# Kernel optimization log

Measured on AMD Instinct MI355X. Metric: run time of the kernel, lower is better.

The kernel has to match this reference:

```python
import jax, jax.numpy as jnp
import numpy as np

EPS = 1e-5


def _bn(x, g, b):
    # training-mode BatchNorm2d over (N, H, W), biased variance
    m = jnp.mean(x, axis=(0, 2, 3), keepdims=True)
    v = jnp.var(x, axis=(0, 2, 3), keepdims=True)
    return (x - m) * jax.lax.rsqrt(v + EPS) * g[None, :, None, None] + b[None, :, None, None]


def _conv1x1(x, w):
    # x: [B, Cin, H, W], w: [Cout, Cin]
    return jnp.einsum('bchw,oc->bohw', x, w)


def _prop_attention(x, wq, wkv, wo, bo, obj_dict, bg_dict, rand_inds):
    B, C, H, W = x.shape  # B == 1
    heads, crop = rand_inds.shape[0], rand_inds.shape[1]
    dh = C // heads
    HW = H * W
    num_obj = crop // 2
    # original does x.clone().detach() before attention
    xd = jax.lax.stop_gradient(x)
    xh = xd.reshape(heads, dh, HW)  # batch=1 folded away (matches t.view(-1, crop**2))
    # pos[h, i, j] = flat pixel index gathered for head h, group i, slot j
    pos = jnp.concatenate(
        [obj_dict[rand_inds[:, :num_obj]], bg_dict[rand_inds[:, num_obj:]]], axis=1
    )  # [heads, crop, crop]
    tokens = jax.vmap(lambda xv, pv: xv[:, pv])(xh, pos)  # [heads, dh, crop, crop]
    tokens = tokens.transpose(0, 2, 3, 1).reshape(heads * crop, crop, dh)
    q = tokens @ wq.T
    k, v = jnp.split(tokens @ wkv.T, 2, axis=-1)
    dots = jnp.einsum('bie,bje->bij', q, k) * (dh ** -0.5)
    attn = jax.nn.softmax(dots, axis=-1)
    out = jnp.einsum('bij,bje->bie', attn, v)  # [heads*crop, crop, dh]
    # faithful to torch out.view(heads*crop, -1, crop): a raw row-major reinterpret
    out_r = out.reshape(heads, crop, dh, crop)
    vals = out_r.transpose(0, 2, 1, 3).reshape(heads, dh, crop * crop)
    pos_flat = pos.reshape(heads, crop * crop)
    # pos is a bijection onto [0, HW) per head -> invert and gather
    ar = jnp.arange(HW, dtype=jnp.int32)
    inv = jax.vmap(lambda p: jnp.zeros((HW,), jnp.int32).at[p].set(ar))(pos_flat)
    img = jax.vmap(lambda vh, ih: vh[:, ih])(vals, inv)  # [heads, dh, HW]
    img = img.reshape(1, heads * dh, H, W)
    # to_out: Linear(dim, dim) applied channels-last
    return jnp.einsum('bchw,oc->bohw', img, wo) + bo[None, :, None, None]


def setup_inputs():
    H = W = 300
    HW = H * W
    heads, crop = 2, H
    num_obj = crop // 2
    ch, emb = 256, 64
    dh = emb // heads
    key = jax.random.key(0)
    ks = jax.random.split(key, 10)
    x = jax.random.normal(ks[0], (1, ch, H, W), jnp.float32)
    perm = jax.random.permutation(ks[1], HW)
    obj_dict = perm[: HW // 2]
    bg_dict = perm[HW // 2 :]
    ri = []
    for h in range(heads):
        po = jax.random.permutation(jax.random.fold_in(ks[2], h), HW // 2).reshape(num_obj, crop)
        pb = jax.random.permutation(jax.random.fold_in(ks[3], h), HW // 2).reshape(crop - num_obj, crop)
        ri.append(jnp.concatenate([po, pb], axis=0))
    rand_inds = jnp.stack(ri)  # [heads, crop, crop]
    w_conv1 = jax.random.normal(ks[4], (emb, ch), jnp.float32) / np.sqrt(ch)
    wq = jax.random.normal(ks[5], (dh, dh), jnp.float32) / np.sqrt(dh)
    wkv = jax.random.normal(ks[6], (2 * dh, dh), jnp.float32) / np.sqrt(dh)
    wo = jax.random.normal(ks[7], (emb, emb), jnp.float32) / np.sqrt(emb)
    bo = jnp.zeros((emb,), jnp.float32)
    w_conv2 = jax.random.normal(ks[8], (emb, 2 * emb), jnp.float32) / np.sqrt(2 * emb)
    return {
        'x': x,
        'w_conv1': w_conv1,
        'bn1_g': jnp.ones((emb,), jnp.float32),
        'bn1_b': jnp.zeros((emb,), jnp.float32),
        'wq': wq,
        'wkv': wkv,
        'wo': wo,
        'bo': bo,
        'w_conv2': w_conv2,
        'bn2_g': jnp.ones((emb,), jnp.float32),
        'bn2_b': jnp.zeros((emb,), jnp.float32),
        'obj_dict': obj_dict,
        'bg_dict': bg_dict,
        'rand_inds': rand_inds,
    }


def reference(x, w_conv1, bn1_g, bn1_b, wq, wkv, wo, bo, w_conv2, bn2_g, bn2_b, obj_dict, bg_dict, rand_inds):
    x1 = jax.nn.relu(_bn(_conv1x1(x, w_conv1), bn1_g, bn1_b))
    xa = jax.nn.relu(_prop_attention(x1, wq, wkv, wo, bo, obj_dict, bg_dict, rand_inds))
    xc = jnp.concatenate([xa, x1], axis=1)
    return jax.nn.relu(_bn(_conv1x1(xc, w_conv2), bn2_g, bn2_b))
```

## Files before the change

kernel.cpp:

```cpp
#include <hip/hip_runtime.h>
#include <hip/hip_bf16.h>

#define HW 90000
#define CROP 300
#define C2EXP 0.25503492f

typedef __attribute__((ext_vector_type(8))) short s8v;
typedef __attribute__((ext_vector_type(4))) float f4v;
#define MFMA16(a,b,c) __builtin_amdgcn_mfma_f32_16x16x32_bf16(a,b,c,0,0,0)

__device__ __forceinline__ unsigned short f2bf(float f) {
    unsigned int u = __float_as_uint(f);
    return (unsigned short)((u + 0x7fffu + ((u >> 16) & 1u)) >> 16);
}
__device__ __forceinline__ float bf2f(unsigned short s) {
    return __uint_as_float(((unsigned int)s) << 16);
}
__device__ __forceinline__ s8v pack8(float4 u0, float4 u1) {
    s8v A;
    A[0] = (short)f2bf(u0.x); A[1] = (short)f2bf(u0.y);
    A[2] = (short)f2bf(u0.z); A[3] = (short)f2bf(u0.w);
    A[4] = (short)f2bf(u1.x); A[5] = (short)f2bf(u1.y);
    A[6] = (short)f2bf(u1.z); A[7] = (short)f2bf(u1.w);
    return A;
}

__global__ void prep_kernel(const float* __restrict__ w1, const float* __restrict__ wq,
                            const float* __restrict__ wkv, const float* __restrict__ wo,
                            const float* __restrict__ w2,
                            short* __restrict__ w1b, short* __restrict__ wqb,
                            short* __restrict__ wkvb, short* __restrict__ wob,
                            short* __restrict__ w2b) {
    int idx = blockIdx.x * blockDim.x + threadIdx.x;
    int stride = gridDim.x * blockDim.x;
    for (int i = idx; i < 16384; i += stride) w1b[i] = (short)f2bf(w1[i]);
    for (int i = idx; i < 1024; i += stride)  wqb[i] = (short)f2bf(wq[i]);
    for (int i = idx; i < 2048; i += stride)  wkvb[i] = (short)f2bf(wkv[i]);
    for (int i = idx; i < 4096; i += stride)  wob[i] = (short)f2bf(wo[i]);
    for (int i = idx; i < 8192; i += stride)  w2b[i] = (short)f2bf(w2[i]);
}

__global__ __launch_bounds__(256, 2) void conv1_mfma(const float* __restrict__ x,
        const short* __restrict__ w1b, float* __restrict__ y1t, float* __restrict__ stat) {
    const int wave = threadIdx.x >> 6, lane = threadIdx.x & 63;
    const int q = lane >> 4, n = lane & 15;
    const int tile = blockIdx.x * 4 + wave;
    const int s0 = tile * 16;
    s8v B[8][4];
#pragma unroll
    for (int kb = 0; kb < 8; ++kb)
#pragma unroll
        for (int nt = 0; nt < 4; ++nt)
            B[kb][nt] = *(const s8v*)(w1b + (nt * 16 + n) * 256 + kb * 32 + q * 8);
    f4v acc[4];
#pragma unroll
    for (int nt = 0; nt < 4; ++nt) acc[nt] = f4v{0.f, 0.f, 0.f, 0.f};
    if (s0 < HW) {
#pragma unroll
        for (int kb = 0; kb < 8; ++kb) {
            float a8[8];
#pragma unroll
            for (int j = 0; j < 8; ++j)
                a8[j] = x[(size_t)(kb * 32 + q * 8 + j) * HW + s0 + n];
            s8v A;
#pragma unroll
            for (int j = 0; j < 8; ++j) A[j] = (short)f2bf(a8[j]);
#pragma unroll
            for (int nt = 0; nt < 4; ++nt) acc[nt] = MFMA16(A, B[kb][nt], acc[nt]);
        }
#pragma unroll
        for (int nt = 0; nt < 4; ++nt)
#pragma unroll
            for (int r = 0; r < 4; ++r)
                y1t[(size_t)(s0 + q * 4 + r) * 64 + nt * 16 + n] = acc[nt][r];
    }
    float s1[4], s2[4];
#pragma unroll
    for (int nt = 0; nt < 4; ++nt) {
        s1[nt] = acc[nt][0] + acc[nt][1] + acc[nt][2] + acc[nt][3];
        s2[nt] = acc[nt][0]*acc[nt][0] + acc[nt][1]*acc[nt][1]
               + acc[nt][2]*acc[nt][2] + acc[nt][3]*acc[nt][3];
    }
#pragma unroll
    for (int m = 16; m < 64; m <<= 1)
#pragma unroll
        for (int nt = 0; nt < 4; ++nt) {
            s1[nt] += __shfl_xor(s1[nt], m, 64);
            s2[nt] += __shfl_xor(s2[nt], m, 64);
        }
    __shared__ float red[2][4][64];
    if (lane < 16)
#pragma unroll
        for (int nt = 0; nt < 4; ++nt) {
            red[0][wave][nt * 16 + lane] = s1[nt];
            red[1][wave][nt * 16 + lane] = s2[nt];
        }
    __syncthreads();
    if (threadIdx.x < 128) {
        int k = threadIdx.x >> 6, c = threadIdx.x & 63;
        atomicAdd(&stat[k * 64 + c],
                  red[k][0][c] + red[k][1][c] + red[k][2][c] + red[k][3][c]);
    }
}

__global__ void bn_fin_kernel(const float* __restrict__ stat,
        const float* __restrict__ g, const float* __restrict__ b, float* __restrict__ ab) {
    int c = threadIdx.x;
    float m = stat[c] * (1.f / HW);
    float v = stat[64 + c] * (1.f / HW) - m * m;
    float ac = g[c] * rsqrtf(v + 1e-5f);
    ab[c] = ac;
    ab[64 + c] = b[c] - m * ac;
}

__global__ __launch_bounds__(512, 4) void attn_mfma_kernel(const float* __restrict__ y1t,
        const float* __restrict__ ab1,
        const short* __restrict__ wqb, const short* __restrict__ wkvb,
        const int* __restrict__ obj, const int* __restrict__ bg,
        const int* __restrict__ rinds, float* __restrict__ img) {
    __shared__ __align__(16) short tokQ[304 * 40];
    __shared__ __align__(16) short kbuf[304 * 40];
    __shared__ __align__(16) short vt[32 * 328];
    __shared__ __align__(16) short pbuf[8 * 16 * 40];
    __shared__ int possh[304];
    const int b = blockIdx.x;
    const int h = b / CROP, i = b - h * CROP;
    const int tid = threadIdx.x;
    const int wave = tid >> 6, lane = tid & 63, q = lane >> 4, n = lane & 15;

    const float4 a4 = *(const float4*)(ab1 + h * 32 + (tid & 7) * 4);
    const float4 b4 = *(const float4*)(ab1 + 64 + h * 32 + (tid & 7) * 4);

    if (tid < 300) {
        int ri = rinds[h * HW + i * CROP + tid];
        possh[tid] = (i < 150) ? obj[ri] : bg[ri];
    } else if (tid < 380) {
        ((unsigned int*)(tokQ + 300 * 40))[tid - 300] = 0;
    } else if (tid < 460) {
        ((unsigned int*)(kbuf + 300 * 40))[tid - 380] = 0;
    }
    for (int ii = tid; ii < 320; ii += 512) {
        int e = ii / 10, w = ii - 10 * e;
        ((unsigned int*)vt)[e * 164 + 150 + w] = 0;
    }
    __syncthreads();

    for (int idx = tid; idx < 2400; idx += 512) {
        int j = idx >> 3, part = idx & 7;
        float4 v = *(const float4*)(y1t + (size_t)possh[j] * 64 + h * 32 + part * 4);
        v.x = fmaxf(fmaf(a4.x, v.x, b4.x), 0.f);
        v.y = fmaxf(fmaf(a4.y, v.y, b4.y), 0.f);
        v.z = fmaxf(fmaf(a4.z, v.z, b4.z), 0.f);
        v.w = fmaxf(fmaf(a4.w, v.w, b4.w), 0.f);
        uint2 pk;
        pk.x = (unsigned int)f2bf(v.x) | ((unsigned int)f2bf(v.y) << 16);
        pk.y = (unsigned int)f2bf(v.z) | ((unsigned int)f2bf(v.w) << 16);
        *(uint2*)(tokQ + j * 40 + part * 4) = pk;
    }
    __syncthreads();

    {
        s8v bq0 = *(const s8v*)(wqb + n * 32 + q * 8);
        s8v bq1 = *(const s8v*)(wqb + (16 + n) * 32 + q * 8);
        s8v bk0 = *(const s8v*)(wkvb + n * 32 + q * 8);
        s8v bk1 = *(const s8v*)(wkvb + (16 + n) * 32 + q * 8);
        s8v bv0 = *(const s8v*)(wkvb + (32 + n) * 32 + q * 8);
        s8v bv1 = *(const s8v*)(wkvb + (48 + n) * 32 + q * 8);
        f4v zz = {0.f, 0.f, 0.f, 0.f};
#pragma unroll
        for (int ti = 0; ti < 3; ++ti) {
            int t = wave + ti * 8;
            if (t < 19) {
                s8v at = *(const s8v*)(tokQ + (16 * t + n) * 40 + q * 8);
                f4v qf0 = MFMA16(at, bq0, zz);
                f4v qf1 = MFMA16(at, bq1, zz);
                f4v kf0 = MFMA16(at, bk0, zz);
                f4v kf1 = MFMA16(at, bk1, zz);
                f4v vf0 = MFMA16(at, bv0, zz);
                f4v vf1 = MFMA16(at, bv1, zz);
#pragma unroll
                for (int r = 0; r < 4; ++r) {
                    int row = 16 * t + q * 4 + r;
                    tokQ[row * 40 + n]      = (short)f2bf(qf0[r]);
                    tokQ[row * 40 + 16 + n] = (short)f2bf(qf1[r]);
                    kbuf[row * 40 + n]      = (short)f2bf(kf0[r]);
                    kbuf[row * 40 + 16 + n] = (short)f2bf(kf1[r]);
                    vt[n * 328 + row]        = (short)f2bf(vf0[r]);
                    vt[(16 + n) * 328 + row] = (short)f2bf(vf1[r]);
                }
            }
        }
    }
    __syncthreads();

    s8v aQ[3];
#pragma unroll
    for (int ti = 0; ti < 3; ++ti) {
        int t = wave + ti * 8;
        aQ[ti] = (t < 19) ? *(const s8v*)(tokQ + (16 * t + n) * 40 + q * 8) : s8v{};
    }
    __syncthreads();

    f4v O[3][2];
    float lsum[3][4];
#pragma unroll
    for (int ti = 0; ti < 3; ++ti) {
        O[ti][0] = f4v{0.f, 0.f, 0.f, 0.f};
        O[ti][1] = f4v{0.f, 0.f, 0.f, 0.f};
#pragma unroll
        for (int r = 0; r < 4; ++r) lsum[ti][r] = 0.f;
    }
    short* pw = pbuf + wave * 16 * 40;
    f4v zz = {0.f, 0.f, 0.f, 0.f};
    for (int kb = 0; kb < 10; ++kb) {
        const int key0 = kb * 32 + n;
        const int key1 = kb * 32 + 16 + n;
        s8v bV0 = *(const s8v*)(vt + n * 328 + kb * 32 + q * 8);
        s8v bV1 = *(const s8v*)(vt + (16 + n) * 328 + kb * 32 + q * 8);
        s8v bK0 = *(const s8v*)(kbuf + key0 * 40 + q * 8);
        int r1 = key1 < 304 ? key1 : 303;
        s8v bK1 = *(const s8v*)(kbuf + r1 * 40 + q * 8);
#pragma unroll
        for (int ti = 0; ti < 3; ++ti) {
            int t = wave + ti * 8;
            if (t >= 19) continue;
            f4v s0 = MFMA16(aQ[ti], bK0, zz);
            f4v s1 = MFMA16(aQ[ti], bK1, zz);
#pragma unroll
            for (int r = 0; r < 4; ++r) {
                float e0 = (key0 < 300) ? exp2f(s0[r] * C2EXP) : 0.f;
                float e1 = (key1 < 300) ? exp2f(s1[r] * C2EXP) : 0.f;
                unsigned short p0 = f2bf(e0), p1 = f2bf(e1);
                lsum[ti][r] += bf2f(p0) + bf2f(p1);
                pw[(q * 4 + r) * 40 + n]      = (short)p0;
                pw[(q * 4 + r) * 40 + 16 + n] = (short)p1;
            }
            asm volatile("s_waitcnt lgkmcnt(0)" ::: "memory");
            s8v ap = *(const s8v*)(pw + n * 40 + q * 8);
            O[ti][0] = MFMA16(ap, bV0, O[ti][0]);
            O[ti][1] = MFMA16(ap, bV1, O[ti][1]);
        }
    }

#pragma unroll
    for (int m = 1; m < 16; m <<= 1) {
#pragma unroll
        for (int ti = 0; ti < 3; ++ti)
#pragma unroll
            for (int r = 0; r < 4; ++r)
                lsum[ti][r] += __shfl_xor(lsum[ti][r], m, 64);
    }
    short* outb = tokQ;
#pragma unroll
    for (int ti = 0; ti < 3; ++ti) {
        int t = wave + ti * 8;
        if (t >= 19) continue;
#pragma unroll
        for (int r = 0; r < 4; ++r) {
            float rl = 1.f / lsum[ti][r];
            int row = 16 * t + q * 4 + r;
            outb[row * 32 + n]      = (short)f2bf(O[ti][0][r] * rl);
            outb[row * 32 + 16 + n] = (short)f2bf(O[ti][1][r] * rl);
        }
    }
    __syncthreads();

    for (int idx = tid; idx < 9600; idx += 512) {
        int jj = idx >> 5, dd = idx & 31;
        img[(size_t)possh[jj] * 64 + h * 32 + dd] = bf2f((unsigned short)outb[dd * CROP + jj]);
    }
}

__global__ __launch_bounds__(256, 2) void fuse2_mfma(const float* __restrict__ img,
        const float* __restrict__ y1t, const float* __restrict__ ab1,
        const short* __restrict__ wob, const short* __restrict__ w2b,
        const float* __restrict__ bo, float* __restrict__ y2, float* __restrict__ stat) {
    __shared__ __align__(16) short xas[4][16 * 72];
    __shared__ float ytr[64 * 133];
    __shared__ float red[2][4][64];
    const int wave = threadIdx.x >> 6, lane = threadIdx.x & 63;
    const int q = lane >> 4, n = lane & 15;
    s8v Bo[2][4], B2[4][4];
#pragma unroll
    for (int kb = 0; kb < 2; ++kb)
#pragma unroll
        for (int nt = 0; nt < 4; ++nt)
            Bo[kb][nt] = *(const s8v*)(wob + (nt * 16 + n) * 64 + kb * 32 + q * 8);
#pragma unroll
    for (int kb = 0; kb < 4; ++kb)
#pragma unroll
        for (int nt = 0; nt < 4; ++nt)
            B2[kb][nt] = *(const s8v*)(w2b + (nt * 16 + n) * 128 + kb * 32 + q * 8);
    float4 a1v[2][2], b1v[2][2];
#pragma unroll
    for (int kb = 0; kb < 2; ++kb)
#pragma unroll
        for (int hh = 0; hh < 2; ++hh) {
            a1v[kb][hh] = *(const float4*)(ab1 + kb * 32 + q * 8 + hh * 4);
            b1v[kb][hh] = *(const float4*)(ab1 + 64 + kb * 32 + q * 8 + hh * 4);
        }
    float bov[4];
#pragma unroll
    for (int nt = 0; nt < 4; ++nt) bov[nt] = bo[nt * 16 + n];

    float s1[4] = {0.f, 0.f, 0.f, 0.f}, s2[4] = {0.f, 0.f, 0.f, 0.f};
    short* xw = xas[wave];
#pragma unroll
    for (int ti = 0; ti < 2; ++ti) {
        int tile = blockIdx.x * 8 + wave * 2 + ti;
        if (tile >= 5625) continue;
        int s0 = tile * 16;
        f4v xacc[4];
#pragma unroll
        for (int nt = 0; nt < 4; ++nt) xacc[nt] = f4v{0.f, 0.f, 0.f, 0.f};
#pragma unroll
        for (int kb = 0; kb < 2; ++kb) {
            const float4* ip = (const float4*)(img + (size_t)(s0 + n) * 64 + kb * 32 + q * 8);
            s8v A = pack8(ip[0], ip[1]);
#pragma unroll
            for (int nt = 0; nt < 4; ++nt) xacc[nt] = MFMA16(A, Bo[kb][nt], xacc[nt]);
        }
#pragma unroll
        for (int nt = 0; nt < 4; ++nt)
#pragma unroll
            for (int r = 0; r < 4; ++r) {
                float v = fmaxf(xacc[nt][r] + bov[nt], 0.f);
                xw[(q * 4 + r) * 72 + nt * 16 + n] = (short)f2bf(v);
            }
        asm volatile("s_waitcnt lgkmcnt(0)" ::: "memory");
        f4v yacc[4];
#pragma unroll
        for (int nt = 0; nt < 4; ++nt) yacc[nt] = f4v{0.f, 0.f, 0.f, 0.f};
#pragma unroll
        for (int kb = 0; kb < 2; ++kb) {
            s8v Axa = *(const s8v*)(xw + n * 72 + kb * 32 + q * 8);
#pragma unroll
            for (int nt = 0; nt < 4; ++nt) yacc[nt] = MFMA16(Axa, B2[kb][nt], yacc[nt]);
        }
#pragma unroll
        for (int kb = 0; kb < 2; ++kb) {
            const float4* yp = (const float4*)(y1t + (size_t)(s0 + n) * 64 + kb * 32 + q * 8);
            float4 u0 = yp[0], u1 = yp[1];
            u0.x = fmaxf(fmaf(a1v[kb][0].x, u0.x, b1v[kb][0].x), 0.f);
            u0.y = fmaxf(fmaf(a1v[kb][0].y, u0.y, b1v[kb][0].y), 0.f);
            u0.z = fmaxf(fmaf(a1v[kb][0].z, u0.z, b1v[kb][0].z), 0.f);
            u0.w = fmaxf(fmaf(a1v[kb][0].w, u0.w, b1v[kb][0].w), 0.f);
            u1.x = fmaxf(fmaf(a1v[kb][1].x, u1.x, b1v[kb][1].x), 0.f);
            u1.y = fmaxf(fmaf(a1v[kb][1].y, u1.y, b1v[kb][1].y), 0.f);
            u1.z = fmaxf(fmaf(a1v[kb][1].z, u1.z, b1v[kb][1].z), 0.f);
            u1.w = fmaxf(fmaf(a1v[kb][1].w, u1.w, b1v[kb][1].w), 0.f);
            s8v A = pack8(u0, u1);
#pragma unroll
            for (int nt = 0; nt < 4; ++nt) yacc[nt] = MFMA16(A, B2[kb + 2][nt], yacc[nt]);
        }
        int pl = wave * 32 + ti * 16;
#pragma unroll
        for (int nt = 0; nt < 4; ++nt)
#pragma unroll
            for (int r = 0; r < 4; ++r) {
                float v = yacc[nt][r];
                s1[nt] += v; s2[nt] += v * v;
                ytr[(nt * 16 + n) * 133 + pl + q * 4 + r] = v;
            }
    }
#pragma unroll
    for (int m = 16; m < 64; m <<= 1)
#pragma unroll
        for (int nt = 0; nt < 4; ++nt) {
            s1[nt] += __shfl_xor(s1[nt], m, 64);
            s2[nt] += __shfl_xor(s2[nt], m, 64);
        }
    if (lane < 16)
#pragma unroll
        for (int nt = 0; nt < 4; ++nt) {
            red[0][wave][nt * 16 + lane] = s1[nt];
            red[1][wave][nt * 16 + lane] = s2[nt];
        }
    __syncthreads();
    int s0b = blockIdx.x * 128;
    for (int i = threadIdx.x; i < 8192; i += 256) {
        int c = i >> 7, p = i & 127;
        int s = s0b + p;
        if (s < HW) y2[(size_t)c * HW + s] = ytr[c * 133 + p];
    }
    if (threadIdx.x < 128) {
        int k = threadIdx.x >> 6, c = threadIdx.x & 63;
        atomicAdd(&stat[k * 64 + c],
                  red[k][0][c] + red[k][1][c] + red[k][2][c] + red[k][3][c]);
    }
}

__global__ __launch_bounds__(256) void bn_out_kernel(const float* __restrict__ y2,
        const float* __restrict__ ab2, float* __restrict__ out) {
    int c = blockIdx.y;
    int s4 = blockIdx.x * 256 + threadIdx.x;
    if (s4 >= 22500) return;
    float a = ab2[c], b = ab2[64 + c];
    float4 v = *(const float4*)(y2 + (size_t)c * HW + s4 * 4);
    v.x = fmaxf(fmaf(a, v.x, b), 0.f);
    v.y = fmaxf(fmaf(a, v.y, b), 0.f);
    v.z = fmaxf(fmaf(a, v.z, b), 0.f);
    v.w = fmaxf(fmaf(a, v.w, b), 0.f);
    *(float4*)(out + (size_t)c * HW + s4 * 4) = v;
}

extern "C" void kernel_launch(void* const* d_in, const int* in_sizes, int n_in,
                              void* d_out, int out_size, void* d_ws, size_t ws_size,
                              hipStream_t stream) {
    const float* x   = (const float*)d_in[0];
    const float* w1  = (const float*)d_in[1];
    const float* g1  = (const float*)d_in[2];
    const float* b1  = (const float*)d_in[3];
    const float* wq  = (const float*)d_in[4];
    const float* wkv = (const float*)d_in[5];
    const float* wo  = (const float*)d_in[6];
    const float* bo  = (const float*)d_in[7];
    const float* w2  = (const float*)d_in[8];
    const float* g2  = (const float*)d_in[9];
    const float* b2  = (const float*)d_in[10];
    const int* obj   = (const int*)d_in[11];
    const int* bg    = (const int*)d_in[12];
    const int* rinds = (const int*)d_in[13];

    short* W1B  = (short*)d_ws;
    short* WOB  = W1B + 16384;
    short* W2B  = WOB + 4096;
    short* WQB  = W2B + 8192;
    short* WKVB = WQB + 1024;
    float* STAT = (float*)d_ws + 16384;
    float* AB1  = STAT + 256;
    float* AB2  = AB1 + 128;
    float* Y1T  = AB2 + 128;
    float* IMG  = Y1T + 5760000;
    float* Y2   = IMG + 5760000;

    hipMemsetAsync(STAT, 0, 1024, stream);
    prep_kernel<<<16, 256, 0, stream>>>(w1, wq, wkv, wo, w2, W1B, WQB, WKVB, WOB, W2B);
    conv1_mfma<<<1408, 256, 0, stream>>>(x, W1B, Y1T, STAT);
    bn_fin_kernel<<<1, 64, 0, stream>>>(STAT, g1, b1, AB1);
    attn_mfma_kernel<<<600, 512, 0, stream>>>(Y1T, AB1, WQB, WKVB, obj, bg, rinds, IMG);
    fuse2_mfma<<<704, 256, 0, stream>>>(IMG, Y1T, AB1, WOB, W2B, bo, Y2, STAT + 128);
    bn_fin_kernel<<<1, 64, 0, stream>>>(STAT + 128, g2, b2, AB2);
    bn_out_kernel<<<dim3(88, 64), 256, 0, stream>>>(Y2, AB2, (float*)d_out);
}
```

Measured before the change: 292.9 us.

## Store conv1 output and intermediates as bf16, add separate BN-ReLU pass, retile conv1

Conv1 now stages its weights in LDS, processes four 16-pixel sub-tiles per wave with float4 loads of x and register prefetch of the next K block, and writes pre-BN activations as bf16 instead of fp32. A new elementwise kernel applies BN1+ReLU once and writes a bf16 x1 buffer. The attention and fuse2 kernels then read bf16 directly, so their gathers and stores are half as wide and they no longer redo the BN math. The cost is an extra launch and an extra full pass over x1, plus bf16 rounding of pre-BN values, which the BN statistics now see in a different precision path.

Result: faster. 265.5 us (-9.3%).

```diff
diff --git a/kernel.cpp b/kernel.cpp
--- a/kernel.cpp
+++ b/kernel.cpp
@@ -15,6 +15,12 @@
 }
 __device__ __forceinline__ float bf2f(unsigned short s) {
     return __uint_as_float(((unsigned int)s) << 16);
+}
+__device__ __forceinline__ unsigned pk_trunc(float a, float b) {
+    return __builtin_amdgcn_perm(__float_as_uint(b), __float_as_uint(a), 0x07060302u);
+}
+__device__ __forceinline__ unsigned pk_rne(float a, float b) {
+    return (unsigned)f2bf(a) | ((unsigned)f2bf(b) << 16);
 }
 __device__ __forceinline__ s8v pack8(float4 u0, float4 u1) {
     s8v A;
@@ -41,46 +47,75 @@
 }
 
 __global__ __launch_bounds__(256, 2) void conv1_mfma(const float* __restrict__ x,
-        const short* __restrict__ w1b, float* __restrict__ y1t, float* __restrict__ stat) {
+        const short* __restrict__ w1b, short* __restrict__ y1b, float* __restrict__ stat) {
+    __shared__ __align__(16) short lw[16384];
+    __shared__ float red[2][4][64];
     const int wave = threadIdx.x >> 6, lane = threadIdx.x & 63;
     const int q = lane >> 4, n = lane & 15;
-    const int tile = blockIdx.x * 4 + wave;
-    const int s0 = tile * 16;
-    s8v B[8][4];
-#pragma unroll
-    for (int kb = 0; kb < 8; ++kb)
-#pragma unroll
-        for (int nt = 0; nt < 4; ++nt)
-            B[kb][nt] = *(const s8v*)(w1b + (nt * 16 + n) * 256 + kb * 32 + q * 8);
-    f4v acc[4];
-#pragma unroll
-    for (int nt = 0; nt < 4; ++nt) acc[nt] = f4v{0.f, 0.f, 0.f, 0.f};
-    if (s0 < HW) {
-#pragma unroll
-        for (int kb = 0; kb < 8; ++kb) {
-            float a8[8];
+    for (int i = threadIdx.x; i < 2048; i += 256)
+        ((uint4*)lw)[i] = ((const uint4*)w1b)[i];
+    __syncthreads();
+
+    const int s0 = blockIdx.x * 256 + wave * 64;
+    const int pb = (s0 + 4 * n <= HW - 4) ? (s0 + 4 * n) : (HW - 4);
+    f4v acc[4][4];
+#pragma unroll
+    for (int mt = 0; mt < 4; ++mt)
+#pragma unroll
+        for (int nt = 0; nt < 4; ++nt) acc[mt][nt] = f4v{0.f, 0.f, 0.f, 0.f};
+
+    float4 cur[8], nxt[8];
+#pragma unroll
+    for (int j = 0; j < 8; ++j)
+        cur[j] = *(const float4*)(x + (size_t)(q * 8 + j) * HW + pb);
+#pragma unroll
+    for (int kb = 0; kb < 8; ++kb) {
+        if (kb < 7) {
 #pragma unroll
             for (int j = 0; j < 8; ++j)
-                a8[j] = x[(size_t)(kb * 32 + q * 8 + j) * HW + s0 + n];
-            s8v A;
-#pragma unroll
-            for (int j = 0; j < 8; ++j) A[j] = (short)f2bf(a8[j]);
-#pragma unroll
-            for (int nt = 0; nt < 4; ++nt) acc[nt] = MFMA16(A, B[kb][nt], acc[nt]);
-        }
-#pragma unroll
-        for (int nt = 0; nt < 4; ++nt)
-#pragma unroll
-            for (int r = 0; r < 4; ++r)
-                y1t[(size_t)(s0 + q * 4 + r) * 64 + nt * 16 + n] = acc[nt][r];
-    }
-    float s1[4], s2[4];
-#pragma unroll
-    for (int nt = 0; nt < 4; ++nt) {
-        s1[nt] = acc[nt][0] + acc[nt][1] + acc[nt][2] + acc[nt][3];
-        s2[nt] = acc[nt][0]*acc[nt][0] + acc[nt][1]*acc[nt][1]
-               + acc[nt][2]*acc[nt][2] + acc[nt][3]*acc[nt][3];
-    }
+                nxt[j] = *(const float4*)(x + (size_t)((kb + 1) * 32 + q * 8 + j) * HW + pb);
+        }
+        s8v A[4];
+#pragma unroll
+        for (int mt = 0; mt < 4; ++mt) {
+            union { unsigned u[4]; s8v v; } am;
+#pragma unroll
+            for (int w = 0; w < 4; ++w)
+                am.u[w] = pk_trunc(((const float*)&cur[2 * w])[mt],
+                                   ((const float*)&cur[2 * w + 1])[mt]);
+            A[mt] = am.v;
+        }
+#pragma unroll
+        for (int mt = 0; mt < 4; ++mt)
+#pragma unroll
+            for (int nt = 0; nt < 4; ++nt) {
+                int c = (nt & 1) + 2 * n + 32 * (nt >> 1);
+                s8v B = *(const s8v*)(lw + c * 256 + kb * 32 + q * 8);
+                acc[mt][nt] = MFMA16(A[mt], B, acc[mt][nt]);
+            }
+        if (kb < 7) {
+#pragma unroll
+            for (int j = 0; j < 8; ++j) cur[j] = nxt[j];
+        }
+    }
+
+    float s1[4] = {0.f, 0.f, 0.f, 0.f}, s2[4] = {0.f, 0.f, 0.f, 0.f};
+#pragma unroll
+    for (int mt = 0; mt < 4; ++mt)
+#pragma unroll
+        for (int r = 0; r < 4; ++r) {
+            int p = s0 + 4 * (q * 4 + r) + mt;
+            if (p < HW) {
+                float v0 = acc[mt][0][r], v1 = acc[mt][1][r];
+                float v2 = acc[mt][2][r], v3 = acc[mt][3][r];
+                *(unsigned*)(y1b + (size_t)p * 64 + 2 * n)      = pk_rne(v0, v1);
+                *(unsigned*)(y1b + (size_t)p * 64 + 32 + 2 * n) = pk_rne(v2, v3);
+                s1[0] += v0; s2[0] += v0 * v0;
+                s1[1] += v1; s2[1] += v1 * v1;
+                s1[2] += v2; s2[2] += v2 * v2;
+                s1[3] += v3; s2[3] += v3 * v3;
+            }
+        }
 #pragma unroll
     for (int m = 16; m < 64; m <<= 1)
 #pragma unroll
@@ -88,12 +123,12 @@
             s1[nt] += __shfl_xor(s1[nt], m, 64);
             s2[nt] += __shfl_xor(s2[nt], m, 64);
         }
-    __shared__ float red[2][4][64];
     if (lane < 16)
 #pragma unroll
         for (int nt = 0; nt < 4; ++nt) {
-            red[0][wave][nt * 16 + lane] = s1[nt];
-            red[1][wave][nt * 16 + lane] = s2[nt];
+            int c = (nt & 1) + 2 * lane + 32 * (nt >> 1);
+            red[0][wave][c] = s1[nt];
+            red[1][wave][c] = s2[nt];
         }
     __syncthreads();
     if (threadIdx.x < 128) {
@@ -113,11 +148,32 @@
     ab[64 + c] = b[c] - m * ac;
 }
 
-__global__ __launch_bounds__(512, 4) void attn_mfma_kernel(const float* __restrict__ y1t,
-        const float* __restrict__ ab1,
+__global__ __launch_bounds__(256) void bnrelu_kernel(const short* __restrict__ y1b,
+        const float* __restrict__ ab1, short* __restrict__ x1b) {
+    int t = blockIdx.x * 256 + threadIdx.x;
+    if (t >= 720000) return;
+    int cb = 8 * (t & 7);
+    float4 a0 = *(const float4*)(ab1 + cb), a1 = *(const float4*)(ab1 + cb + 4);
+    float4 b0 = *(const float4*)(ab1 + 64 + cb), b1 = *(const float4*)(ab1 + 64 + cb + 4);
+    uint4 u = ((const uint4*)y1b)[t];
+    float r0 = fmaxf(fmaf(a0.x, __uint_as_float(u.x << 16), b0.x), 0.f);
+    float r1 = fmaxf(fmaf(a0.y, __uint_as_float(u.x & 0xffff0000u), b0.y), 0.f);
+    float r2 = fmaxf(fmaf(a0.z, __uint_as_float(u.y << 16), b0.z), 0.f);
+    float r3 = fmaxf(fmaf(a0.w, __uint_as_float(u.y & 0xffff0000u), b0.w), 0.f);
+    float r4 = fmaxf(fmaf(a1.x, __uint_as_float(u.z << 16), b1.x), 0.f);
+    float r5 = fmaxf(fmaf(a1.y, __uint_as_float(u.z & 0xffff0000u), b1.y), 0.f);
+    float r6 = fmaxf(fmaf(a1.z, __uint_as_float(u.w << 16), b1.z), 0.f);
+    float r7 = fmaxf(fmaf(a1.w, __uint_as_float(u.w & 0xffff0000u), b1.w), 0.f);
+    uint4 o;
+    o.x = pk_rne(r0, r1); o.y = pk_rne(r2, r3);
+    o.z = pk_rne(r4, r5); o.w = pk_rne(r6, r7);
+    ((uint4*)x1b)[t] = o;
+}
+
+__global__ __launch_bounds__(512, 4) void attn_mfma_kernel(const short* __restrict__ x1b,
         const short* __restrict__ wqb, const short* __restrict__ wkvb,
         const int* __restrict__ obj, const int* __restrict__ bg,
-        const int* __restrict__ rinds, float* __restrict__ img) {
+        const int* __restrict__ rinds, short* __restrict__ imgb) {
     __shared__ __align__(16) short tokQ[304 * 40];
     __shared__ __align__(16) short kbuf[304 * 40];
     __shared__ __align__(16) short vt[32 * 328];
@@ -128,9 +184,6 @@
     const int tid = threadIdx.x;
     const int wave = tid >> 6, lane = tid & 63, q = lane >> 4, n = lane & 15;
 
-    const float4 a4 = *(const float4*)(ab1 + h * 32 + (tid & 7) * 4);
-    const float4 b4 = *(const float4*)(ab1 + 64 + h * 32 + (tid & 7) * 4);
-
     if (tid < 300) {
         int ri = rinds[h * HW + i * CROP + tid];
         possh[tid] = (i < 150) ? obj[ri] : bg[ri];
@@ -145,17 +198,10 @@
     }
     __syncthreads();
 
-    for (int idx = tid; idx < 2400; idx += 512) {
-        int j = idx >> 3, part = idx & 7;
-        float4 v = *(const float4*)(y1t + (size_t)possh[j] * 64 + h * 32 + part * 4);
-        v.x = fmaxf(fmaf(a4.x, v.x, b4.x), 0.f);
-        v.y = fmaxf(fmaf(a4.y, v.y, b4.y), 0.f);
-        v.z = fmaxf(fmaf(a4.z, v.z, b4.z), 0.f);
-        v.w = fmaxf(fmaf(a4.w, v.w, b4.w), 0.f);
-        uint2 pk;
-        pk.x = (unsigned int)f2bf(v.x) | ((unsigned int)f2bf(v.y) << 16);
-        pk.y = (unsigned int)f2bf(v.z) | ((unsigned int)f2bf(v.w) << 16);
-        *(uint2*)(tokQ + j * 40 + part * 4) = pk;
+    for (int idx = tid; idx < 1200; idx += 512) {
+        int j = idx >> 2, part = idx & 3;
+        *(uint4*)(tokQ + j * 40 + part * 8) =
+            *(const uint4*)(x1b + (size_t)possh[j] * 64 + h * 32 + part * 8);
     }
     __syncthreads();
 
@@ -267,12 +313,12 @@
 
     for (int idx = tid; idx < 9600; idx += 512) {
         int jj = idx >> 5, dd = idx & 31;
-        img[(size_t)possh[jj] * 64 + h * 32 + dd] = bf2f((unsigned short)outb[dd * CROP + jj]);
-    }
-}
-
-__global__ __launch_bounds__(256, 2) void fuse2_mfma(const float* __restrict__ img,
-        const float* __restrict__ y1t, const float* __restrict__ ab1,
+        imgb[(size_t)possh[jj] * 64 + h * 32 + dd] = outb[dd * CROP + jj];
+    }
+}
+
+__global__ __launch_bounds__(256, 2) void fuse2_mfma(const short* __restrict__ imgb,
+        const short* __restrict__ x1b,
         const short* __restrict__ wob, const short* __restrict__ w2b,
         const float* __restrict__ bo, float* __restrict__ y2, float* __restrict__ stat) {
     __shared__ __align__(16) short xas[4][16 * 72];
@@ -291,14 +337,6 @@
 #pragma unroll
         for (int nt = 0; nt < 4; ++nt)
             B2[kb][nt] = *(const s8v*)(w2b + (nt * 16 + n) * 128 + kb * 32 + q * 8);
-    float4 a1v[2][2], b1v[2][2];
-#pragma unroll
-    for (int kb = 0; kb < 2; ++kb)
-#pragma unroll
-        for (int hh = 0; hh < 2; ++hh) {
-            a1v[kb][hh] = *(const float4*)(ab1 + kb * 32 + q * 8 + hh * 4);
-            b1v[kb][hh] = *(const float4*)(ab1 + 64 + kb * 32 + q * 8 + hh * 4);
-        }
     float bov[4];
 #pragma unroll
     for (int nt = 0; nt < 4; ++nt) bov[nt] = bo[nt * 16 + n];
@@ -315,8 +353,7 @@
         for (int nt = 0; nt < 4; ++nt) xacc[nt] = f4v{0.f, 0.f, 0.f, 0.f};
 #pragma unroll
         for (int kb = 0; kb < 2; ++kb) {
-            const float4* ip = (const float4*)(img + (size_t)(s0 + n) * 64 + kb * 32 + q * 8);
-            s8v A = pack8(ip[0], ip[1]);
+            s8v A = *(const s8v*)(imgb + (size_t)(s0 + n) * 64 + kb * 32 + q * 8);
 #pragma unroll
             for (int nt = 0; nt < 4; ++nt) xacc[nt] = MFMA16(A, Bo[kb][nt], xacc[nt]);
         }
@@ -339,17 +376,7 @@
         }
 #pragma unroll
         for (int kb = 0; kb < 2; ++kb) {
-            const float4* yp = (const float4*)(y1t + (size_t)(s0 + n) * 64 + kb * 32 + q * 8);
-            float4 u0 = yp[0], u1 = yp[1];
-            u0.x = fmaxf(fmaf(a1v[kb][0].x, u0.x, b1v[kb][0].x), 0.f);
-            u0.y = fmaxf(fmaf(a1v[kb][0].y, u0.y, b1v[kb][0].y), 0.f);
-            u0.z = fmaxf(fmaf(a1v[kb][0].z, u0.z, b1v[kb][0].z), 0.f);
-            u0.w = fmaxf(fmaf(a1v[kb][0].w, u0.w, b1v[kb][0].w), 0.f);
-            u1.x = fmaxf(fmaf(a1v[kb][1].x, u1.x, b1v[kb][1].x), 0.f);
-            u1.y = fmaxf(fmaf(a1v[kb][1].y, u1.y, b1v[kb][1].y), 0.f);
-            u1.z = fmaxf(fmaf(a1v[kb][1].z, u1.z, b1v[kb][1].z), 0.f);
-            u1.w = fmaxf(fmaf(a1v[kb][1].w, u1.w, b1v[kb][1].w), 0.f);
-            s8v A = pack8(u0, u1);
+            s8v A = *(const s8v*)(x1b + (size_t)(s0 + n) * 64 + kb * 32 + q * 8);
 #pragma unroll
             for (int nt = 0; nt < 4; ++nt) yacc[nt] = MFMA16(A, B2[kb + 2][nt], yacc[nt]);
         }
@@ -422,24 +449,27 @@
     const int* bg    = (const int*)d_in[12];
     const int* rinds = (const int*)d_in[13];
 
+    float* WSF  = (float*)d_ws;
     short* W1B  = (short*)d_ws;
     short* WOB  = W1B + 16384;
     short* W2B  = WOB + 4096;
     short* WQB  = W2B + 8192;
     short* WKVB = WQB + 1024;
-    float* STAT = (float*)d_ws + 16384;
+    float* STAT = WSF + 16384;
     float* AB1  = STAT + 256;
     float* AB2  = AB1 + 128;
-    float* Y1T  = AB2 + 128;
-    float* IMG  = Y1T + 5760000;
-    float* Y2   = IMG + 5760000;
+    short* Y1B  = (short*)(WSF + 16896);
+    short* X1B  = Y1B + 5760000;
+    short* IMGB = X1B + 5760000;
+    float* Y2   = WSF + 16896 + 8640000;
 
     hipMemsetAsync(STAT, 0, 1024, stream);
     prep_kernel<<<16, 256, 0, stream>>>(w1, wq, wkv, wo, w2, W1B, WQB, WKVB, WOB, W2B);
-    conv1_mfma<<<1408, 256, 0, stream>>>(x, W1B, Y1T, STAT);
+    conv1_mfma<<<352, 256, 0, stream>>>(x, W1B, Y1B, STAT);
     bn_fin_kernel<<<1, 64, 0, stream>>>(STAT, g1, b1, AB1);
-    attn_mfma_kernel<<<600, 512, 0, stream>>>(Y1T, AB1, WQB, WKVB, obj, bg, rinds, IMG);
-    fuse2_mfma<<<704, 256, 0, stream>>>(IMG, Y1T, AB1, WOB, W2B, bo, Y2, STAT + 128);
+    bnrelu_kernel<<<2813, 256, 0, stream>>>(Y1B, AB1, X1B);
+    attn_mfma_kernel<<<600, 512, 0, stream>>>(X1B, WQB, WKVB, obj, bg, rinds, IMGB);
+    fuse2_mfma<<<704, 256, 0, stream>>>(IMGB, X1B, WOB, W2B, bo, Y2, STAT + 128);
     bn_fin_kernel<<<1, 64, 0, stream>>>(STAT + 128, g2, b2, AB2);
     bn_out_kernel<<<dim3(88, 64), 256, 0, stream>>>(Y2, AB2, (float*)d_out);
 }
```
